# Kernel tuning notes

Measured on AMD Instinct MI355X. Metric: run time of the kernel, lower is better.

The kernel has to match this reference:

```python
import jax, jax.numpy as jnp
import numpy as np

B, L, D = 4, 2048, 2048
H, KVH = 16, 4
HD = D // H            # 128
G = H // KVH           # GQA group size
K_SEL = L // 4         # top_k_ratio = 0.25 -> 512
MAX_SEQ = 8192
THETA = 10000.0
SCALE = HD ** -0.5
NEG = -1e9


def _rope_tables(dim, max_len, theta):
    inv = 1.0 / theta ** (jnp.arange(0, dim, 2, dtype=jnp.float32) / dim)  # (dim/2,)
    ang = jnp.arange(max_len, dtype=jnp.float32)[:, None] * inv[None, :]   # (max_len, dim/2)
    return jnp.cos(ang), jnp.sin(ang)


def _apply_rope_pos(x, cos, sin, pos):
    # x: (B, h, K, HD), pos: (B, K) int positions
    c = cos[pos][:, None]  # (B,1,K,HD/2)
    s = sin[pos][:, None]
    x1, x2 = jnp.split(x, 2, axis=-1)
    return jnp.concatenate([x1 * c - x2 * s, x1 * s + x2 * c], axis=-1)


def setup_inputs() -> dict:
    key = jax.random.key(0)
    ks = jax.random.split(key, 8)
    std = 0.02
    x   = jax.random.normal(ks[0], (B, L, D), dtype=jnp.float32)
    Wq  = jax.random.normal(ks[1], (D, D), dtype=jnp.float32) * std
    Wkv = jax.random.normal(ks[2], (D, 2 * KVH * HD), dtype=jnp.float32) * std
    Wo  = jax.random.normal(ks[3], (D, D), dtype=jnp.float32) * std
    W1  = jax.random.normal(ks[4], (D, D // 4), dtype=jnp.float32) * std
    b1  = jnp.zeros((D // 4,), dtype=jnp.float32)
    W2  = jax.random.normal(ks[5], (D // 4, 1), dtype=jnp.float32) * std
    b2  = jnp.zeros((1,), dtype=jnp.float32)
    return {"x": x, "Wq": Wq, "Wkv": Wkv, "Wo": Wo,
            "W1": W1, "b1": b1, "W2": W2, "b2": b2}


def reference(x, Wq, Wkv, Wo, W1, b1, W2, b2):
    Bx, Lx, Dx = x.shape
    # 1. learned per-token importance scores
    imp = (jax.nn.gelu(x @ W1 + b1, approximate=False) @ W2 + b2)[..., 0]  # (B,L)
    # 2. top-k token selection, sorted to keep original order
    _, idx = jax.lax.top_k(imp, K_SEL)
    idx = jnp.sort(idx, axis=-1)                                           # (B,K)
    x_sel = jnp.take_along_axis(x, idx[..., None], axis=1)                 # (B,K,D)
    # 3. fused KV projection on the selected subset (GQA)
    kv = x_sel @ Wkv
    k, v = jnp.split(kv, 2, axis=-1)
    k = k.reshape(Bx, K_SEL, KVH, HD).transpose(0, 2, 1, 3)                # (B,KVH,K,HD)
    v = v.reshape(Bx, K_SEL, KVH, HD).transpose(0, 2, 1, 3)
    # 4. RoPE with original positions for K, contiguous positions for Q
    cos, sin = _rope_tables(HD, MAX_SEQ, THETA)
    k = _apply_rope_pos(k, cos, sin, idx)
    q = (x @ Wq).reshape(Bx, Lx, H, HD).transpose(0, 2, 1, 3)              # (B,H,L,HD)
    qpos = jnp.broadcast_to(jnp.arange(Lx)[None, :], (Bx, Lx))
    q = _apply_rope_pos(q, cos, sin, qpos)
    # 5. GQA head expansion + attention over gathered keys
    k = jnp.repeat(k, G, axis=1)                                           # (B,H,K,HD)
    v = jnp.repeat(v, G, axis=1)
    scores = jnp.einsum('bhld,bhkd->bhlk', q, k) * SCALE                   # (B,H,L,K)
    # causal mask on original key positions
    causal = idx[:, None, None, :] > jnp.arange(Lx)[None, None, :, None]
    scores = jnp.where(causal, NEG, scores)
    attn = jax.nn.softmax(scores, axis=-1)
    # 6. importance soft gating (gradient path into the scorer)
    gate = jax.nn.sigmoid(jnp.take_along_axis(imp, idx, axis=1))           # (B,K)
    attn = attn * gate[:, None, None, :]
    out = jnp.einsum('bhlk,bhkd->bhld', attn, v)                           # (B,H,L,HD)
    out = out.transpose(0, 2, 1, 3).reshape(Bx, Lx, Dx)
    return out @ Wo
```

## Files before the change

### kernel.cpp

```cpp
#include <hip/hip_runtime.h>
#include <math.h>

typedef unsigned short u16;
typedef __attribute__((ext_vector_type(8))) short short8;
typedef __attribute__((ext_vector_type(4))) float f32x4;

__device__ __forceinline__ float bf2f(u16 u) {
  return __uint_as_float(((unsigned)u) << 16);
}
__device__ __forceinline__ u16 f2bf(float f) {
  unsigned u = __float_as_uint(f);
  return (u16)((u + 0x7fffu + ((u >> 16) & 1u)) >> 16);
}

__device__ __forceinline__ void gload_lds16(const u16* g, u16* l) {
  __builtin_amdgcn_global_load_lds((const __attribute__((address_space(1))) unsigned int*)g,
                                   (__attribute__((address_space(3))) unsigned int*)l, 16, 0, 0);
}

__device__ __forceinline__ void stage_tile(const u16* __restrict__ gbase, int ldg,
                                           u16* lds, int w, int lane) {
  #pragma unroll
  for (int i = 0; i < 4; ++i) {
    int c = w * 4 + i;
    const u16* g = gbase + (size_t)(c * 8 + (lane >> 3)) * ldg + (lane & 7) * 8;
    gload_lds16(g, lds + c * 512);
  }
}

__global__ __launch_bounds__(256) void cvt_x_kernel(const float* __restrict__ x,
                                                    u16* __restrict__ xb,
                                                    u16* __restrict__ xlo) {
  size_t base = ((size_t)blockIdx.x * 256 + threadIdx.x) * 8;
  short8 hi, lo;
  #pragma unroll
  for (int i = 0; i < 8; ++i) {
    float v = x[base + i];
    u16 h = f2bf(v);
    hi[i] = (short)h;
    lo[i] = (short)f2bf(v - bf2f(h));
  }
  *(short8*)&xb[base] = hi;
  *(short8*)&xlo[base] = lo;
}

template <bool HILO>
__global__ __launch_bounds__(256) void transpose_cvt(const float* __restrict__ in,
                                                     u16* __restrict__ outH,
                                                     u16* __restrict__ outL,
                                                     int R, int C) {
  __shared__ u16 tH[64][72];
  __shared__ u16 tL[64][72];
  int rb = blockIdx.y * 64, cb = blockIdx.x * 64;
  int t = threadIdx.x;
  #pragma unroll
  for (int i = 0; i < 16; ++i) {
    int r = i * 4 + (t >> 6), c = t & 63;
    float v = in[(size_t)(rb + r) * C + cb + c];
    u16 h = f2bf(v);
    tH[r][c] = h;
    if (HILO) tL[r][c] = f2bf(v - bf2f(h));
  }
  __syncthreads();
  #pragma unroll
  for (int i = 0; i < 16; ++i) {
    int r = i * 4 + (t >> 6), c = t & 63;
    outH[(size_t)(cb + r) * R + rb + c] = tH[c][r];
    if (HILO) outL[(size_t)(cb + r) * R + rb + c] = tL[c][r];
  }
}

__global__ void ropetab_kernel(float* __restrict__ cosT, float* __restrict__ sinT) {
  int pos = blockIdx.x, i = threadIdx.x;
  float e = (float)(2 * i) * (1.0f / 128.0f);
  float inv = powf(10000.0f, -e);
  float ang = (float)pos * inv;
  cosT[pos * 64 + i] = cosf(ang);
  sinT[pos * 64 + i] = sinf(ang);
}

template <bool BF16OUT>
__global__ __launch_bounds__(512, 2) void gemm256(const u16* __restrict__ A,
                                                  const u16* __restrict__ BT,
                                                  float* __restrict__ Cf,
                                                  u16* __restrict__ Cb,
                                                  int M, int N, int K) {
  __shared__ __align__(1024) u16 smem[65536];
  const int bm = blockIdx.x * 256, bn = blockIdx.y * 256;
  const int t = threadIdx.x, lane = t & 63, w = t >> 6;
  const int ll = lane & 15, lh = lane >> 4;
  const int wr = w >> 2, wc = w & 3;
  const int NT = K >> 6;

  const int tt0 = t, tt1 = t + 512;
  const int r0 = tt0 >> 2, r1 = tt1 >> 2;
  const int c0 = (((tt0 & 3) ^ ((tt0 >> 3) & 3)) << 3);
  const int c1 = (((tt1 & 3) ^ ((tt1 >> 3) & 3)) << 3);
  const size_t aoff0 = (size_t)(bm + r0) * K + c0;
  const size_t aoff1 = (size_t)(bm + r1) * K + c1;
  const size_t boff0 = (size_t)(bn + r0) * K + c0;
  const size_t boff1 = (size_t)(bn + r1) * K + c1;

  const int swz = ((lh ^ ((ll >> 1) & 3)) << 3);
  const int arow = (wr * 128 + ll) * 32 + swz;
  const int brow = (wc * 64 + ll) * 32 + swz;

  f32x4 acc[8][4];
  #pragma unroll
  for (int mi = 0; mi < 8; ++mi)
    #pragma unroll
    for (int ni = 0; ni < 4; ++ni) acc[mi][ni] = f32x4{0.f, 0.f, 0.f, 0.f};

  short8 aq[8], bq[2];

#define G_STAGE(base, o0, o1, lds) \
  gload_lds16((base) + (o0), (lds) + w * 512); \
  gload_lds16((base) + (o1), (lds) + 4096 + w * 512)
#define RD_A(Sa, ks) \
  _Pragma("unroll") for (int mi = 0; mi < 8; ++mi) aq[mi] = *(const short8*)&(Sa)[(ks)*8192 + arow + mi * 512]
#define RD_B(Sb, ks, nh) \
  _Pragma("unroll") for (int n2 = 0; n2 < 2; ++n2) bq[n2] = *(const short8*)&(Sb)[(ks)*8192 + brow + ((nh)*2 + n2) * 512]
#define DO_MFMA(nh) \
  __builtin_amdgcn_s_setprio(1); \
  _Pragma("unroll") for (int mi = 0; mi < 8; ++mi) \
    _Pragma("unroll") for (int n2 = 0; n2 < 2; ++n2) \
      acc[mi][(nh)*2 + n2] = __builtin_amdgcn_mfma_f32_16x16x32_bf16(aq[mi], bq[n2], acc[mi][(nh)*2 + n2], 0, 0, 0); \
  __builtin_amdgcn_s_setprio(0)
#define VMW(n) asm volatile("s_waitcnt vmcnt(" #n ")" ::: "memory")

  G_STAGE(A, aoff0, aoff1, smem);
  G_STAGE(BT, boff0, boff1, smem + 16384);
  G_STAGE(A, aoff0 + 32, aoff1 + 32, smem + 8192);
  G_STAGE(BT, boff0 + 32, boff1 + 32, smem + 16384 + 8192);

  for (int kt = 0; kt < NT - 1; ++kt) {
    const int cur = kt & 1;
    u16* Sa = smem + cur * 32768;
    u16* Sb = Sa + 16384;
    u16* Pa = smem + (cur ^ 1) * 32768;
    u16* Pb = Pa + 16384;
    const size_t kg = (size_t)(kt + 1) * 64;
    VMW(4);
    __builtin_amdgcn_s_barrier();
    G_STAGE(A, aoff0 + kg, aoff1 + kg, Pa);
    RD_A(Sa, 0);
    RD_B(Sb, 0, 0);
    DO_MFMA(0);
    G_STAGE(BT, boff0 + kg, boff1 + kg, Pb);
    RD_B(Sb, 0, 1);
    DO_MFMA(1);
    VMW(4);
    __builtin_amdgcn_s_barrier();
    G_STAGE(A, aoff0 + kg + 32, aoff1 + kg + 32, Pa + 8192);
    RD_A(Sa, 1);
    RD_B(Sb, 1, 0);
    DO_MFMA(0);
    G_STAGE(BT, boff0 + kg + 32, boff1 + kg + 32, Pb + 8192);
    RD_B(Sb, 1, 1);
    DO_MFMA(1);
  }
  {
    const int cur = (NT - 1) & 1;
    u16* Sa = smem + cur * 32768;
    u16* Sb = Sa + 16384;
    VMW(4);
    __builtin_amdgcn_s_barrier();
    RD_A(Sa, 0); RD_B(Sb, 0, 0); DO_MFMA(0);
    RD_B(Sb, 0, 1); DO_MFMA(1);
    VMW(0);
    __builtin_amdgcn_s_barrier();
    RD_A(Sa, 1); RD_B(Sb, 1, 0); DO_MFMA(0);
    RD_B(Sb, 1, 1); DO_MFMA(1);
  }

  #pragma unroll
  for (int mi = 0; mi < 8; ++mi)
    #pragma unroll
    for (int ni = 0; ni < 4; ++ni)
      #pragma unroll
      for (int r = 0; r < 4; ++r) {
        int row = bm + wr * 128 + mi * 16 + lh * 4 + r;
        int col = bn + wc * 64 + ni * 16 + ll;
        float v = acc[mi][ni][r];
        if (BF16OUT) Cb[(size_t)row * N + col] = f2bf(v);
        else Cf[(size_t)row * N + col] = v;
      }
#undef G_STAGE
#undef RD_A
#undef RD_B
#undef DO_MFMA
#undef VMW
}

__global__ __launch_bounds__(256) void gemm_bt_gather(const u16* __restrict__ A,
                                                      const u16* __restrict__ BT,
                                                      const int* __restrict__ rowidx,
                                                      u16* __restrict__ Cb,
                                                      int M, int N, int K) {
  constexpr int BK = 64;
  __shared__ u16 As[128][BK + 8];
  __shared__ u16 Bs[128][BK + 8];
  const int bm = blockIdx.x * 128, bn = blockIdx.y * 128;
  const int t = threadIdx.x, lane = t & 63, w = t >> 6;
  const int lh = lane >> 4, ll = lane & 15;
  const int wm = (w >> 1) * 64, wn = (w & 1) * 64;
  f32x4 acc[4][4];
  #pragma unroll
  for (int mt = 0; mt < 4; ++mt)
    #pragma unroll
    for (int nt = 0; nt < 4; ++nt) acc[mt][nt] = f32x4{0.f, 0.f, 0.f, 0.f};

  for (int kb = 0; kb < K; kb += BK) {
    __syncthreads();
    #pragma unroll
    for (int i = 0; i < 4; ++i) {
      int e = t + i * 256;
      int row = e >> 3, c8 = e & 7;
      int arow = rowidx[bm + row];
      *(short8*)&As[row][c8 * 8] = *(const short8*)&A[(size_t)arow * K + kb + c8 * 8];
      *(short8*)&Bs[row][c8 * 8] = *(const short8*)&BT[(size_t)(bn + row) * K + kb + c8 * 8];
    }
    __syncthreads();
    #pragma unroll
    for (int ks = 0; ks < 2; ++ks) {
      short8 a[4], b[4];
      #pragma unroll
      for (int mt = 0; mt < 4; ++mt) a[mt] = *(const short8*)&As[wm + mt * 16 + ll][ks * 32 + lh * 8];
      #pragma unroll
      for (int nt = 0; nt < 4; ++nt) b[nt] = *(const short8*)&Bs[wn + nt * 16 + ll][ks * 32 + lh * 8];
      #pragma unroll
      for (int mt = 0; mt < 4; ++mt)
        #pragma unroll
        for (int nt = 0; nt < 4; ++nt)
          acc[mt][nt] = __builtin_amdgcn_mfma_f32_16x16x32_bf16(a[mt], b[nt], acc[mt][nt], 0, 0, 0);
    }
  }
  #pragma unroll
  for (int mt = 0; mt < 4; ++mt)
    #pragma unroll
    for (int nt = 0; nt < 4; ++nt)
      #pragma unroll
      for (int r = 0; r < 4; ++r) {
        int row = bm + wm + mt * 16 + lh * 4 + r;
        int col = bn + wn + nt * 16 + ll;
        Cb[(size_t)row * N + col] = f2bf(acc[mt][nt][r]);
      }
}

__global__ __launch_bounds__(256) void gemm_scorer(const u16* __restrict__ Ahi,
                                                   const u16* __restrict__ Alo,
                                                   const u16* __restrict__ Bhi,
                                                   const u16* __restrict__ Blo,
                                                   float* __restrict__ Cpart,
                                                   int M, int N, int K) {
  __shared__ __align__(1024) u16 smem[4 * 128 * 64];
  u16* AsH = smem;
  u16* AsL = smem + 128 * 64;
  u16* BsH = smem + 2 * 128 * 64;
  u16* BsL = smem + 3 * 128 * 64;
  const int bm = blockIdx.x * 128, bn = blockIdx.y * 128;
  const int kz = blockIdx.z;
  const int t = threadIdx.x, lane = t & 63, w = t >> 6;
  const int lh = lane >> 4, ll = lane & 15;
  const int wm = (w >> 1) * 64, wn = (w & 1) * 64;
  f32x4 acc[4][4];
  #pragma unroll
  for (int mt = 0; mt < 4; ++mt)
    #pragma unroll
    for (int nt = 0; nt < 4; ++nt) acc[mt][nt] = f32x4{0.f, 0.f, 0.f, 0.f};

  const int k0 = kz * (K / 2), k1 = k0 + K / 2;
  for (int kb = k0; kb < k1; kb += 64) {
    __syncthreads();
    stage_tile(Ahi + (size_t)bm * K + kb, K, AsH, w, lane);
    stage_tile(Alo + (size_t)bm * K + kb, K, AsL, w, lane);
    stage_tile(Bhi + (size_t)bn * K + kb, K, BsH, w, lane);
    stage_tile(Blo + (size_t)bn * K + kb, K, BsL, w, lane);
    __syncthreads();
    #pragma unroll
    for (int ks = 0; ks < 2; ++ks) {
      short8 ah[4], al[4], bh[4], bl[4];
      #pragma unroll
      for (int mt = 0; mt < 4; ++mt) {
        int o = (wm + mt * 16 + ll) * 64 + ks * 32 + lh * 8;
        ah[mt] = *(const short8*)&AsH[o];
        al[mt] = *(const short8*)&AsL[o];
      }
      #pragma unroll
      for (int nt = 0; nt < 4; ++nt) {
        int o = (wn + nt * 16 + ll) * 64 + ks * 32 + lh * 8;
        bh[nt] = *(const short8*)&BsH[o];
        bl[nt] = *(const short8*)&BsL[o];
      }
      #pragma unroll
      for (int mt = 0; mt < 4; ++mt)
        #pragma unroll
        for (int nt = 0; nt < 4; ++nt) {
          acc[mt][nt] = __builtin_amdgcn_mfma_f32_16x16x32_bf16(ah[mt], bh[nt], acc[mt][nt], 0, 0, 0);
          acc[mt][nt] = __builtin_amdgcn_mfma_f32_16x16x32_bf16(ah[mt], bl[nt], acc[mt][nt], 0, 0, 0);
          acc[mt][nt] = __builtin_amdgcn_mfma_f32_16x16x32_bf16(al[mt], bh[nt], acc[mt][nt], 0, 0, 0);
        }
    }
  }
  float* C = Cpart + (size_t)kz * M * N;
  #pragma unroll
  for (int mt = 0; mt < 4; ++mt)
    #pragma unroll
    for (int nt = 0; nt < 4; ++nt)
      #pragma unroll
      for (int r = 0; r < 4; ++r) {
        int row = bm + wm + mt * 16 + lh * 4 + r;
        int col = bn + wn + nt * 16 + ll;
        C[(size_t)row * N + col] = acc[mt][nt][r];
      }
}

__global__ __launch_bounds__(256) void scorer_finish(const float* __restrict__ hg,
                                                     const float* __restrict__ b1,
                                                     const float* __restrict__ W2,
                                                     const float* __restrict__ b2,
                                                     float* __restrict__ imp) {
  int tok = blockIdx.x * 4 + (threadIdx.x >> 6);
  int lane = threadIdx.x & 63;
  const float* h0 = hg + (size_t)tok * 512;
  const float* h1 = hg + (size_t)8192 * 512 + (size_t)tok * 512;
  float s = 0.f;
  #pragma unroll
  for (int i = 0; i < 8; ++i) {
    int c = lane + i * 64;
    float v = h0[c] + h1[c] + b1[c];
    v = 0.5f * v * (1.0f + erff(v * 0.70710678118654752f));
    s += v * W2[c];
  }
  #pragma unroll
  for (int off = 32; off; off >>= 1) s += __shfl_xor(s, off, 64);
  if (lane == 0) imp[tok] = s + b2[0];
}

__global__ __launch_bounds__(1024) void topk_kernel(const float* __restrict__ imp,
                                                    int* __restrict__ idx_sel,
                                                    int* __restrict__ sel_rows,
                                                    float* __restrict__ gatev) {
  __shared__ float v[2048];
  __shared__ int ix[2048];
  __shared__ int ids[512];
  int b = blockIdx.x, t = threadIdx.x;
  for (int i = t; i < 2048; i += 1024) { v[i] = imp[b * 2048 + i]; ix[i] = i; }
  __syncthreads();
  for (int k = 2; k <= 2048; k <<= 1)
    for (int j = k >> 1; j > 0; j >>= 1) {
      int i = ((t & ~(j - 1)) << 1) | (t & (j - 1));
      int l2 = i | j;
      bool dir = ((i & k) == 0);
      float vi = v[i], vl = v[l2];
      int xi = ix[i], xl = ix[l2];
      bool g = (vi < vl) || (vi == vl && xi > xl);
      if (g == dir) { v[i] = vl; v[l2] = vi; ix[i] = xl; ix[l2] = xi; }
      __syncthreads();
    }
  if (t < 512) ids[t] = ix[t];
  __syncthreads();
  for (int k = 2; k <= 512; k <<= 1)
    for (int j = k >> 1; j > 0; j >>= 1) {
      if (t < 256) {
        int i = ((t & ~(j - 1)) << 1) | (t & (j - 1));
        int l2 = i | j;
        bool dir = ((i & k) == 0);
        int ai = ids[i], al = ids[l2];
        if ((ai > al) == dir) { ids[i] = al; ids[l2] = ai; }
      }
      __syncthreads();
    }
  if (t < 512) {
    int id = ids[t];
    idx_sel[b * 512 + t] = id;
    sel_rows[b * 512 + t] = b * 2048 + id;
    float g = imp[b * 2048 + id];
    gatev[b * 512 + t] = 1.0f / (1.0f + __expf(-g));
  }
}

__global__ __launch_bounds__(256) void rope_q_kernel(u16* __restrict__ q,
                                                     const float* __restrict__ cosT,
                                                     const float* __restrict__ sinT) {
  int gid = blockIdx.x * 256 + threadIdx.x;
  int i = gid & 63, h = (gid >> 6) & 15;
  int tok = gid >> 10;
  int l = tok & 2047;
  size_t base = (size_t)tok * 2048 + h * 128 + i;
  float q1 = bf2f(q[base]), q2 = bf2f(q[base + 64]);
  float c = cosT[l * 64 + i], s = sinT[l * 64 + i];
  q[base] = f2bf(q1 * c - q2 * s);
  q[base + 64] = f2bf(q1 * s + q2 * c);
}

__global__ __launch_bounds__(256) void rope_k_kernel(const u16* __restrict__ kv,
                                                     const int* __restrict__ idx_sel,
                                                     const float* __restrict__ cosT,
                                                     const float* __restrict__ sinT,
                                                     u16* __restrict__ Kb) {
  int gid = blockIdx.x * 256 + threadIdx.x;
  int i = gid & 63;
  int s = (gid >> 6) & 511;
  int kvh = (gid >> 15) & 3;
  int b = gid >> 17;
  size_t src = (size_t)(b * 512 + s) * 1024 + kvh * 128 + i;
  float k1 = bf2f(kv[src]), k2 = bf2f(kv[src + 64]);
  int pos = idx_sel[b * 512 + s];
  float c = cosT[pos * 64 + i], sn = sinT[pos * 64 + i];
  size_t dst = (size_t)((b * 4 + kvh) * 512 + s) * 128 + i;
  Kb[dst] = f2bf(k1 * c - k2 * sn);
  Kb[dst + 64] = f2bf(k1 * sn + k2 * c);
}

__global__ __launch_bounds__(256) void vtrans_kernel(const u16* __restrict__ kv,
                                                     u16* __restrict__ VT) {
  int gid = blockIdx.x * 256 + threadIdx.x;
  int s = gid & 511;
  int d = (gid >> 9) & 127;
  int kvh = (gid >> 16) & 3;
  int b = gid >> 18;
  VT[(size_t)((b * 4 + kvh) * 128 + d) * 512 + s] =
      kv[(size_t)(b * 512 + s) * 1024 + 512 + kvh * 128 + d];
}

__global__ __launch_bounds__(512) void attn_kernel(const u16* __restrict__ Qb,
                                                   const u16* __restrict__ Kb,
                                                   const u16* __restrict__ VTb,
                                                   const int* __restrict__ idxp,
                                                   const float* __restrict__ gate,
                                                   u16* __restrict__ Ob) {
  __shared__ u16 Ks[64][136];
  __shared__ u16 Vs[128][72];
  __shared__ u16 Ps[8][16][76];
  __shared__ int idx_s[64];
  __shared__ float gate_s[64];

  const int qt = blockIdx.x, h = blockIdx.y, b = blockIdx.z;
  const int kvh = h >> 2;
  const int t = threadIdx.x, lane = t & 63, w = t >> 6;
  const int lh = lane >> 4, ll = lane & 15;
  const int q0 = qt * 128;
  const float SCALE_LOG2E = 0.12753102331f;

  short8 aq[4];
  #pragma unroll
  for (int ks = 0; ks < 4; ++ks)
    aq[ks] = *(const short8*)&Qb[(size_t)(b * 2048 + q0 + w * 16 + ll) * 2048 + h * 128 + ks * 32 + lh * 8];

  float m[4], lden[4];
  f32x4 O[8];
  #pragma unroll
  for (int r = 0; r < 4; ++r) { m[r] = -INFINITY; lden[r] = 0.f; }
  #pragma unroll
  for (int dt = 0; dt < 8; ++dt) O[dt] = f32x4{0.f, 0.f, 0.f, 0.f};

  for (int kt = 0; kt < 8; ++kt) {
    __syncthreads();
    #pragma unroll
    for (int i = 0; i < 2; ++i) {
      int e = t + i * 512;
      int krow = e >> 4, kc8 = e & 15;
      *(short8*)&Ks[krow][kc8 * 8] =
          *(const short8*)&Kb[(size_t)((b * 4 + kvh) * 512 + kt * 64 + krow) * 128 + kc8 * 8];
      int vrow = e >> 3, vc8 = e & 7;
      *(short8*)&Vs[vrow][vc8 * 8] =
          *(const short8*)&VTb[(size_t)((b * 4 + kvh) * 128 + vrow) * 512 + kt * 64 + vc8 * 8];
    }
    if (t < 64) {
      idx_s[t] = idxp[b * 512 + kt * 64 + t];
      gate_s[t] = gate[b * 512 + kt * 64 + t];
    }
    __syncthreads();

    f32x4 S[4];
    #pragma unroll
    for (int nt = 0; nt < 4; ++nt) S[nt] = f32x4{0.f, 0.f, 0.f, 0.f};
    #pragma unroll
    for (int nt = 0; nt < 4; ++nt)
      #pragma unroll
      for (int ks = 0; ks < 4; ++ks) {
        short8 bk = *(const short8*)&Ks[nt * 16 + ll][ks * 32 + lh * 8];
        S[nt] = __builtin_amdgcn_mfma_f32_16x16x32_bf16(aq[ks], bk, S[nt], 0, 0, 0);
      }

    float p[4][4], lmax[4];
    #pragma unroll
    for (int r = 0; r < 4; ++r) lmax[r] = -INFINITY;
    #pragma unroll
    for (int nt = 0; nt < 4; ++nt) {
      int kpos = idx_s[nt * 16 + ll];
      #pragma unroll
      for (int r = 0; r < 4; ++r) {
        int row = q0 + w * 16 + lh * 4 + r;
        float s = S[nt][r] * SCALE_LOG2E;
        if (kpos > row) s = -1e9f;
        p[nt][r] = s;
        lmax[r] = fmaxf(lmax[r], s);
      }
    }
    #pragma unroll
    for (int off = 8; off; off >>= 1)
      #pragma unroll
      for (int r = 0; r < 4; ++r) lmax[r] = fmaxf(lmax[r], __shfl_xor(lmax[r], off, 64));

    bool grow = false;
    #pragma unroll
    for (int r = 0; r < 4; ++r) grow = grow || (lmax[r] > m[r]);
    if (__any(grow)) {
      #pragma unroll
      for (int r = 0; r < 4; ++r) {
        float mnew = fmaxf(m[r], lmax[r]);
        float alpha = exp2f(m[r] - mnew);
        m[r] = mnew;
        lden[r] *= alpha;
        #pragma unroll
        for (int dt = 0; dt < 8; ++dt) O[dt][r] *= alpha;
      }
    }

    float rs[4] = {0.f, 0.f, 0.f, 0.f};
    #pragma unroll
    for (int nt = 0; nt < 4; ++nt)
      #pragma unroll
      for (int r = 0; r < 4; ++r) {
        float e = exp2f(p[nt][r] - m[r]);
        p[nt][r] = e;
        rs[r] += e;
      }
    #pragma unroll
    for (int off = 8; off; off >>= 1)
      #pragma unroll
      for (int r = 0; r < 4; ++r) rs[r] += __shfl_xor(rs[r], off, 64);
    #pragma unroll
    for (int r = 0; r < 4; ++r) lden[r] += rs[r];

    #pragma unroll
    for (int nt = 0; nt < 4; ++nt) {
      float g = gate_s[nt * 16 + ll];
      #pragma unroll
      for (int r = 0; r < 4; ++r) Ps[w][lh * 4 + r][nt * 16 + ll] = f2bf(p[nt][r] * g);
    }
    #pragma unroll
    for (int ks = 0; ks < 2; ++ks) {
      short8 pa = *(const short8*)&Ps[w][ll][ks * 32 + lh * 8];
      #pragma unroll
      for (int dt = 0; dt < 8; ++dt) {
        short8 vb = *(const short8*)&Vs[dt * 16 + ll][ks * 32 + lh * 8];
        O[dt] = __builtin_amdgcn_mfma_f32_16x16x32_bf16(pa, vb, O[dt], 0, 0, 0);
      }
    }
  }

  #pragma unroll
  for (int dt = 0; dt < 8; ++dt)
    #pragma unroll
    for (int r = 0; r < 4; ++r) {
      int row = q0 + w * 16 + lh * 4 + r;
      int col = h * 128 + dt * 16 + ll;
      Ob[(size_t)(b * 2048 + row) * 2048 + col] = f2bf(O[dt][r] / lden[r]);
    }
}

extern "C" void kernel_launch(void* const* d_in, const int* in_sizes, int n_in,
                              void* d_out, int out_size, void* d_ws, size_t ws_size,
                              hipStream_t stream) {
  const float* x = (const float*)d_in[0];
  const float* Wq = (const float*)d_in[1];
  const float* Wkv = (const float*)d_in[2];
  const float* Wo = (const float*)d_in[3];
  const float* W1 = (const float*)d_in[4];
  const float* b1 = (const float*)d_in[5];
  const float* W2 = (const float*)d_in[6];
  const float* b2 = (const float*)d_in[7];
  float* out = (float*)d_out;

  char* ws = (char*)d_ws;
  size_t off = 0;
  auto alloc = [&](size_t bytes) {
    char* p = ws + off;
    off = (off + bytes + 255) & ~(size_t)255;
    return p;
  };
  u16* xb = (u16*)alloc((size_t)8192 * 2048 * 2);
  u16* xlo = (u16*)alloc((size_t)8192 * 2048 * 2);
  u16* W1Th = (u16*)alloc((size_t)512 * 2048 * 2);
  u16* W1Tl = (u16*)alloc((size_t)512 * 2048 * 2);
  u16* WqT = (u16*)alloc((size_t)2048 * 2048 * 2);
  u16* WkvT = (u16*)alloc((size_t)1024 * 2048 * 2);
  u16* WoT = (u16*)alloc((size_t)2048 * 2048 * 2);
  float* cosT = (float*)alloc((size_t)2048 * 64 * 4);
  float* sinT = (float*)alloc((size_t)2048 * 64 * 4);
  float* hg = (float*)alloc((size_t)2 * 8192 * 512 * 4);
  float* impv = (float*)alloc((size_t)8192 * 4);
  int* idx_sel = (int*)alloc((size_t)2048 * 4);
  int* sel_rows = (int*)alloc((size_t)2048 * 4);
  float* gatev = (float*)alloc((size_t)2048 * 4);
  u16* qbuf = (u16*)alloc((size_t)8192 * 2048 * 2);
  u16* kvbuf = (u16*)alloc((size_t)2048 * 1024 * 2);
  u16* Kbuf = (u16*)alloc((size_t)4 * 4 * 512 * 128 * 2);
  u16* VTbuf = (u16*)alloc((size_t)4 * 4 * 128 * 512 * 2);
  u16* attn_out = xlo;

  cvt_x_kernel<<<8192, 256, 0, stream>>>(x, xb, xlo);
  transpose_cvt<true><<<dim3(512 / 64, 2048 / 64), 256, 0, stream>>>(W1, W1Th, W1Tl, 2048, 512);
  transpose_cvt<false><<<dim3(32, 32), 256, 0, stream>>>(Wq, WqT, nullptr, 2048, 2048);
  transpose_cvt<false><<<dim3(16, 32), 256, 0, stream>>>(Wkv, WkvT, nullptr, 2048, 1024);
  transpose_cvt<false><<<dim3(32, 32), 256, 0, stream>>>(Wo, WoT, nullptr, 2048, 2048);
  ropetab_kernel<<<2048, 64, 0, stream>>>(cosT, sinT);

  gemm_scorer<<<dim3(64, 4, 2), 256, 0, stream>>>(xb, xlo, W1Th, W1Tl, hg, 8192, 512, 2048);
  scorer_finish<<<2048, 256, 0, stream>>>(hg, b1, W2, b2, impv);
  topk_kernel<<<4, 1024, 0, stream>>>(impv, idx_sel, sel_rows, gatev);

  gemm256<true><<<dim3(32, 8), 512, 0, stream>>>(xb, WqT, nullptr, qbuf, 8192, 2048, 2048);
  rope_q_kernel<<<32768, 256, 0, stream>>>(qbuf, cosT, sinT);

  gemm_bt_gather<<<dim3(16, 8), 256, 0, stream>>>(xb, WkvT, sel_rows, kvbuf, 2048, 1024, 2048);
  rope_k_kernel<<<2048, 256, 0, stream>>>(kvbuf, idx_sel, cosT, sinT, Kbuf);
  vtrans_kernel<<<4096, 256, 0, stream>>>(kvbuf, VTbuf);

  attn_kernel<<<dim3(16, 16, 4), 512, 0, stream>>>(qbuf, Kbuf, VTbuf, idx_sel, gatev, attn_out);

  gemm256<false><<<dim3(32, 8), 512, 0, stream>>>(attn_out, WoT, out, nullptr, 8192, 2048, 2048);
}
```

Measured before the change: 410.1 us.

## Skip fully-masked key tiles, fold gate into V, lazy softmax rescale

The attention kernel now skips key tiles whose smallest original position lies beyond the query tile. The skip is only taken when the tile's rows see at least one valid key, so rows that would be fully masked keep the reference uniform-softmax behaviour. It also drops the causal mask compare when a whole tile is visible to the warp, and only rescales the running max when it grows by more than 8 (log2 units). The importance gate is folded into V during the transpose kernel, and P is converted with a packed bf16 instruction. Together these cut MFMA, load and exp work in attention, at the cost of slightly different rounding: the gate is applied to V in bf16, and the lazy max threshold can let exponentials exceed 1.

```diff
diff --git a/kernel.cpp b/kernel.cpp
--- a/kernel.cpp
+++ b/kernel.cpp
@@ -414,27 +414,26 @@
 }
 
 __global__ __launch_bounds__(256) void vtrans_kernel(const u16* __restrict__ kv,
+                                                     const float* __restrict__ gatev,
                                                      u16* __restrict__ VT) {
   int gid = blockIdx.x * 256 + threadIdx.x;
   int s = gid & 511;
   int d = (gid >> 9) & 127;
   int kvh = (gid >> 16) & 3;
   int b = gid >> 18;
-  VT[(size_t)((b * 4 + kvh) * 128 + d) * 512 + s] =
-      kv[(size_t)(b * 512 + s) * 1024 + 512 + kvh * 128 + d];
+  float v = bf2f(kv[(size_t)(b * 512 + s) * 1024 + 512 + kvh * 128 + d]);
+  VT[(size_t)((b * 4 + kvh) * 128 + d) * 512 + s] = f2bf(v * gatev[b * 512 + s]);
 }
 
 __global__ __launch_bounds__(512) void attn_kernel(const u16* __restrict__ Qb,
                                                    const u16* __restrict__ Kb,
                                                    const u16* __restrict__ VTb,
                                                    const int* __restrict__ idxp,
-                                                   const float* __restrict__ gate,
                                                    u16* __restrict__ Ob) {
   __shared__ u16 Ks[64][136];
   __shared__ u16 Vs[128][72];
   __shared__ u16 Ps[8][16][76];
   __shared__ int idx_s[64];
-  __shared__ float gate_s[64];
 
   const int qt = blockIdx.x, h = blockIdx.y, b = blockIdx.z;
   const int kvh = h >> 2;
@@ -443,6 +442,8 @@
   const int q0 = qt * 128;
   const float SCALE_LOG2E = 0.12753102331f;
 
+  const bool skipOK = (idxp[b * 512] <= q0);
+
   short8 aq[4];
   #pragma unroll
   for (int ks = 0; ks < 4; ++ks)
@@ -456,6 +457,11 @@
   for (int dt = 0; dt < 8; ++dt) O[dt] = f32x4{0.f, 0.f, 0.f, 0.f};
 
   for (int kt = 0; kt < 8; ++kt) {
+    const int tmin = idxp[b * 512 + kt * 64];
+    if (skipOK && tmin > q0 + 127) continue;
+    const int tmax = idxp[b * 512 + kt * 64 + 63];
+    const bool nomask = (tmax <= q0 + w * 16);
+
     __syncthreads();
     #pragma unroll
     for (int i = 0; i < 2; ++i) {
@@ -467,10 +473,7 @@
       *(short8*)&Vs[vrow][vc8 * 8] =
           *(const short8*)&VTb[(size_t)((b * 4 + kvh) * 128 + vrow) * 512 + kt * 64 + vc8 * 8];
     }
-    if (t < 64) {
-      idx_s[t] = idxp[b * 512 + kt * 64 + t];
-      gate_s[t] = gate[b * 512 + kt * 64 + t];
-    }
+    if (t < 64) idx_s[t] = idxp[b * 512 + kt * 64 + t];
     __syncthreads();
 
     f32x4 S[4];
@@ -487,16 +490,27 @@
     float p[4][4], lmax[4];
     #pragma unroll
     for (int r = 0; r < 4; ++r) lmax[r] = -INFINITY;
-    #pragma unroll
-    for (int nt = 0; nt < 4; ++nt) {
-      int kpos = idx_s[nt * 16 + ll];
-      #pragma unroll
-      for (int r = 0; r < 4; ++r) {
-        int row = q0 + w * 16 + lh * 4 + r;
-        float s = S[nt][r] * SCALE_LOG2E;
-        if (kpos > row) s = -1e9f;
-        p[nt][r] = s;
-        lmax[r] = fmaxf(lmax[r], s);
+    if (nomask) {
+      #pragma unroll
+      for (int nt = 0; nt < 4; ++nt)
+        #pragma unroll
+        for (int r = 0; r < 4; ++r) {
+          float s = S[nt][r] * SCALE_LOG2E;
+          p[nt][r] = s;
+          lmax[r] = fmaxf(lmax[r], s);
+        }
+    } else {
+      #pragma unroll
+      for (int nt = 0; nt < 4; ++nt) {
+        int kpos = idx_s[nt * 16 + ll];
+        #pragma unroll
+        for (int r = 0; r < 4; ++r) {
+          int row = q0 + w * 16 + lh * 4 + r;
+          float s = S[nt][r] * SCALE_LOG2E;
+          if (kpos > row) s = -1e9f;
+          p[nt][r] = s;
+          lmax[r] = fmaxf(lmax[r], s);
+        }
       }
     }
     #pragma unroll
@@ -504,10 +518,10 @@
       #pragma unroll
       for (int r = 0; r < 4; ++r) lmax[r] = fmaxf(lmax[r], __shfl_xor(lmax[r], off, 64));
 
-    bool grow = false;
-    #pragma unroll
-    for (int r = 0; r < 4; ++r) grow = grow || (lmax[r] > m[r]);
-    if (__any(grow)) {
+    bool need = false;
+    #pragma unroll
+    for (int r = 0; r < 4; ++r) need = need || (lmax[r] > m[r] + 8.0f);
+    if (__any(need)) {
       #pragma unroll
       for (int r = 0; r < 4; ++r) {
         float mnew = fmaxf(m[r], lmax[r]);
@@ -536,11 +550,14 @@
     for (int r = 0; r < 4; ++r) lden[r] += rs[r];
 
     #pragma unroll
-    for (int nt = 0; nt < 4; ++nt) {
-      float g = gate_s[nt * 16 + ll];
-      #pragma unroll
-      for (int r = 0; r < 4; ++r) Ps[w][lh * 4 + r][nt * 16 + ll] = f2bf(p[nt][r] * g);
-    }
+    for (int nt = 0; nt < 4; ++nt)
+      #pragma unroll
+      for (int r = 0; r < 4; r += 2) {
+        unsigned pk;
+        asm("v_cvt_pk_bf16_f32 %0, %1, %2" : "=v"(pk) : "v"(p[nt][r]), "v"(p[nt][r + 1]));
+        Ps[w][lh * 4 + r][nt * 16 + ll] = (u16)pk;
+        Ps[w][lh * 4 + r + 1][nt * 16 + ll] = (u16)(pk >> 16);
+      }
     #pragma unroll
     for (int ks = 0; ks < 2; ++ks) {
       short8 pa = *(const short8*)&Ps[w][ll][ks * 32 + lh * 8];
@@ -618,9 +635,9 @@
 
   gemm_bt_gather<<<dim3(16, 8), 256, 0, stream>>>(xb, WkvT, sel_rows, kvbuf, 2048, 1024, 2048);
   rope_k_kernel<<<2048, 256, 0, stream>>>(kvbuf, idx_sel, cosT, sinT, Kbuf);
-  vtrans_kernel<<<4096, 256, 0, stream>>>(kvbuf, VTbuf);
-
-  attn_kernel<<<dim3(16, 16, 4), 512, 0, stream>>>(qbuf, Kbuf, VTbuf, idx_sel, gatev, attn_out);
+  vtrans_kernel<<<4096, 256, 0, stream>>>(kvbuf, gatev, VTbuf);
+
+  attn_kernel<<<dim3(16, 16, 4), 512, 0, stream>>>(qbuf, Kbuf, VTbuf, idx_sel, attn_out);
 
   gemm256<false><<<dim3(32, 8), 512, 0, stream>>>(attn_out, WoT, out, nullptr, 8192, 2048, 2048);
 }
```

Result: no change. 402.6 us (-1.8%).
